# Kernel optimization log

Measured on AMD Instinct MI355X. Metric: run time of the kernel, lower is better.

Reference implementation:

```python
import jax, jax.numpy as jnp
import numpy as np

DIM = 64      # fixed by fuse=BasicConv2d(64,64)
HEADS = 8
B, H, W = 16, 128, 128
CPH = DIM // HEADS  # 8 channels per head


def conv2d(x, w, groups=1, pad=1):
    # x: [B,C,H,W], w: [O, C//groups, kh, kw]
    return jax.lax.conv_general_dilated(
        x, w, window_strides=(1, 1), padding=[(pad, pad), (pad, pad)],
        dimension_numbers=("NCHW", "OIHW", "NCHW"), feature_group_count=groups)


def setup_inputs() -> dict:
    key = jax.random.key(0)
    ks = jax.random.split(key, 8)
    y = jax.random.normal(ks[0], (B, DIM, H, W), jnp.float32)
    # conv3d kernels collapse to their middle depth slice (depth-1 input, zero pad)
    w_qkv = jax.random.normal(ks[1], (3 * DIM, DIM), jnp.float32) * 0.05        # 1x1x1 qkv
    w_dw = jax.random.normal(ks[2], (3 * DIM, 1, 3, 3), jnp.float32) * 0.1      # depthwise 3x3
    w_proj = jax.random.normal(ks[3], (DIM, DIM), jnp.float32) * 0.05           # 1x1x1 project_out
    w_fc = jax.random.normal(ks[4], (9, 3 * HEADS), jnp.float32) * 0.1          # fc: 24->9
    b_fc = jnp.zeros((9,), jnp.float32)
    w_dep = jax.random.normal(ks[5], (DIM, 9, 3, 3), jnp.float32) * 0.1         # grouped: 72->64, groups=8
    b_dep = jnp.zeros((DIM,), jnp.float32)
    temperature = jnp.ones((HEADS, 1, 1), jnp.float32)
    w_fuse = jax.random.normal(ks[6], (DIM, DIM, 3, 3), jnp.float32) * 0.05     # fuse conv, no bias
    bn_gamma = jnp.ones((DIM,), jnp.float32)
    bn_beta = jnp.zeros((DIM,), jnp.float32)
    bn_mean = jnp.zeros((DIM,), jnp.float32)
    bn_var = jnp.ones((DIM,), jnp.float32)
    return dict(y=y, w_qkv=w_qkv, w_dw=w_dw, w_proj=w_proj, w_fc=w_fc, b_fc=b_fc,
                w_dep=w_dep, b_dep=b_dep, temperature=temperature, w_fuse=w_fuse,
                bn_gamma=bn_gamma, bn_beta=bn_beta, bn_mean=bn_mean, bn_var=bn_var)


def reference(y, w_qkv, w_dw, w_proj, w_fc, b_fc, w_dep, b_dep, temperature,
              w_fuse, bn_gamma, bn_beta, bn_mean, bn_var):
    b, c, h, w = y.shape
    # qkv 1x1 conv then 3x3 depthwise conv (groups = 3*DIM)
    qkv = jnp.einsum('oc,bchw->bohw', w_qkv, y)                 # [b,192,h,w]
    qkv = conv2d(qkv, w_dw, groups=3 * DIM, pad=1)
    # dynamic kernel generation branch: flat reshape (row-major, matches torch)
    f_all = qkv.reshape(b, h * w, 3 * HEADS, CPH).transpose(0, 2, 1, 3)  # [b,24,hw,8]
    f_all = jnp.einsum('oc,bcne->bone', w_fc, f_all) + b_fc[None, :, None, None]  # [b,9,hw,8]
    f_conv = f_all.transpose(0, 3, 1, 2).reshape(b, 9 * CPH, h, w)       # [b,72,h,w]
    out_conv = conv2d(f_conv, w_dep, groups=CPH, pad=1) + b_dep[None, :, None, None]
    # channel (transposed) attention with L2-normalize + temperature + softmax
    q, k, v = jnp.split(qkv, 3, axis=1)
    def to_heads(t):
        return t.reshape(b, HEADS, CPH, h * w)
    q, k, v = to_heads(q), to_heads(k), to_heads(v)
    q = q / jnp.maximum(jnp.linalg.norm(q, axis=-1, keepdims=True), 1e-12)
    k = k / jnp.maximum(jnp.linalg.norm(k, axis=-1, keepdims=True), 1e-12)
    attn = jnp.einsum('bhcn,bhdn->bhcd', q, k) * temperature[None]       # [b,8,8,8]
    attn = jax.nn.softmax(attn, axis=-1)
    out = jnp.einsum('bhcd,bhdn->bhcn', attn, v).reshape(b, DIM, h, w)
    out = jnp.einsum('oc,bchw->bohw', w_proj, out)
    output = out + out_conv
    # fuse: conv3x3 (no bias) + BatchNorm (inference stats), then residual + ReLU
    fused = conv2d(output, w_fuse, pad=1)
    scale = (bn_gamma / jnp.sqrt(bn_var + 1e-5))[None, :, None, None]
    fused = (fused - bn_mean[None, :, None, None]) * scale + bn_beta[None, :, None, None]
    return jax.nn.relu(fused + y)
```

## Files before the change

### kernel.cpp

```cpp
#include <hip/hip_runtime.h>
#include <hip/hip_bf16.h>

#define BN 16
#define CC 64
#define HH 128
#define WW 128
#define HW 16384
#define C3 192
#define NHEADS 8


__global__ __launch_bounds__(256) void k_qkv1(const float* __restrict__ y,
                                              const float* __restrict__ w_qkv,
                                              float* __restrict__ out, int chunk) {
    __shared__ float ws[64 * 64];
    int tid = threadIdx.x;
    for (int i = tid; i < 4096; i += 256) {
        int c = i >> 6, o = i & 63;
        ws[i] = w_qkv[(chunk * 64 + o) * 64 + c];
    }
    __syncthreads();
    int bid = blockIdx.x;
    int b = bid >> 6;
    int ptile = bid & 63;
    int pxg = tid & 127;
    int osub = tid >> 7;
    int p0 = ptile * 256 + pxg * 2;
    const float* yb = y + (size_t)b * CC * HW + p0;
    float acc0[32];
    float acc1[32];
#pragma unroll
    for (int o = 0; o < 32; ++o) { acc0[o] = 0.f; acc1[o] = 0.f; }
    for (int c = 0; c < 64; ++c) {
        float2 yv = *(const float2*)(yb + (size_t)c * HW);
        const float* wr = &ws[c * 64 + osub * 32];
#pragma unroll
        for (int o = 0; o < 32; ++o) {
            float w = wr[o];
            acc0[o] = fmaf(w, yv.x, acc0[o]);
            acc1[o] = fmaf(w, yv.y, acc1[o]);
        }
    }
    float* ob = out + (size_t)b * 64 * HW + (size_t)(osub * 32) * HW + p0;
#pragma unroll
    for (int o = 0; o < 32; ++o) {
        *(float2*)(ob + (size_t)o * HW) = make_float2(acc0[o], acc1[o]);
    }
}

__global__ __launch_bounds__(256) void k_dw(const float* __restrict__ in,
                                            const float* __restrict__ w_dw,
                                            float* __restrict__ out, int chunk) {
    int bid = blockIdx.x;
    int tid = threadIdx.x;
    int b = bid >> 11;
    int rem = bid & 2047;
    int ch = rem >> 5;
    int tile = rem & 31;
    int pp = tile * 512 + tid * 2;
    int py = pp >> 7, px = pp & 127;
    const float* ib = in + ((size_t)b * 64 + ch) * HW;
    const float* wr = w_dw + (chunk * 64 + ch) * 9;
    float w[9];
#pragma unroll
    for (int i = 0; i < 9; ++i) w[i] = wr[i];
    float a0 = 0.f, a1 = 0.f;
#pragma unroll
    for (int ky = 0; ky < 3; ++ky) {
        int yy = py + ky - 1;
        bool yok = (unsigned)yy < 128u;
#pragma unroll
        for (int kx = 0; kx < 4; ++kx) {
            int xx = px + kx - 1;
            bool ok = yok && ((unsigned)xx < 128u);
            float v = ok ? ib[yy * 128 + xx] : 0.f;
            if (kx < 3) a0 = fmaf(w[ky * 3 + kx], v, a0);
            if (kx > 0) a1 = fmaf(w[ky * 3 + kx - 1], v, a1);
        }
    }
    *(float2*)(out + ((size_t)b * C3 + chunk * 64 + ch) * HW + pp) = make_float2(a0, a1);
}

__global__ __launch_bounds__(256) void k_fc(const float* __restrict__ qkv,
                                            const float* __restrict__ w_fc,
                                            const float* __restrict__ b_fc,
                                            float* __restrict__ fconv) {
    __shared__ float wf[216];
    __shared__ float bf[9];
    int tid = threadIdx.x;
    if (tid < 216) wf[tid] = w_fc[tid];
    if (tid < 9) bf[tid] = b_fc[tid];
    __syncthreads();
    int bid = blockIdx.x;
    int b = bid >> 9;
    int rem = bid & 511;
    int n = rem * 32 + (tid >> 3);
    int e = tid & 7;
    const float* x = qkv + (size_t)b * C3 * HW + (size_t)n * 192 + e;
    float xe[24];
#pragma unroll
    for (int g = 0; g < 24; ++g) xe[g] = x[g * 8];
    float* ob = fconv + (size_t)b * 72 * HW + n;
#pragma unroll
    for (int o = 0; o < 9; ++o) {
        float acc = bf[o];
#pragma unroll
        for (int g = 0; g < 24; ++g) acc = fmaf(wf[o * 24 + g], xe[g], acc);
        ob[(size_t)(e * 9 + o) * HW] = acc;
    }
}

#define GST 20
__global__ __launch_bounds__(256) void k_gconv(const float* __restrict__ fconv,
                                               const float* __restrict__ w_dep,
                                               const float* __restrict__ b_dep,
                                               float* __restrict__ outO) {
    __shared__ __align__(16) float sm_in[9 * 18 * GST];
    __shared__ __align__(16) float sm_w[81 * 8];
    __shared__ float sm_b[8];
    int tid = threadIdx.x;
    int bid = blockIdx.x;
    int b = bid >> 9;
    int rem = bid & 511;
    int grp = rem >> 6;
    int tile = rem & 63;
    int ty0 = (tile >> 3) * 16, tx0 = (tile & 7) * 16;
    const float* ibase = fconv + ((size_t)b * 72 + grp * 9) * HW;
    for (int i = tid; i < 9 * 324; i += 256) {
        int c = i / 324;
        int r2 = i - c * 324;
        int r = r2 / 18;
        int q = r2 - r * 18;
        int yy = ty0 + r - 1, xx = tx0 + q - 1;
        sm_in[c * (18 * GST) + r * GST + q] =
            ((unsigned)yy < 128u && (unsigned)xx < 128u)
                ? ibase[(size_t)c * HW + yy * 128 + xx] : 0.f;
    }
    for (int i = tid; i < 648; i += 256) {
        int o = i & 7;
        int ik = i >> 3;
        sm_w[i] = w_dep[(size_t)(grp * 8 + o) * 81 + ik];
    }
    if (tid < 8) sm_b[tid] = b_dep[grp * 8 + tid];
    __syncthreads();
    int row = tid >> 4, col = tid & 15;
    float acc[8];
#pragma unroll
    for (int o = 0; o < 8; ++o) acc[o] = sm_b[o];
#pragma unroll
    for (int ic = 0; ic < 9; ++ic) {
        float nb[3][3];
        const float* sc = &sm_in[ic * (18 * GST) + row * GST + col];
#pragma unroll
        for (int r = 0; r < 3; ++r)
#pragma unroll
            for (int q = 0; q < 3; ++q) nb[r][q] = sc[r * GST + q];
        const float* wp = &sm_w[ic * 72];
#pragma unroll
        for (int k = 0; k < 9; ++k) {
            float4 w0 = *(const float4*)(wp + k * 8);
            float4 w1 = *(const float4*)(wp + k * 8 + 4);
            float v = nb[k / 3][k % 3];
            acc[0] = fmaf(w0.x, v, acc[0]);
            acc[1] = fmaf(w0.y, v, acc[1]);
            acc[2] = fmaf(w0.z, v, acc[2]);
            acc[3] = fmaf(w0.w, v, acc[3]);
            acc[4] = fmaf(w1.x, v, acc[4]);
            acc[5] = fmaf(w1.y, v, acc[5]);
            acc[6] = fmaf(w1.z, v, acc[6]);
            acc[7] = fmaf(w1.w, v, acc[7]);
        }
    }
    float* ob = outO + ((size_t)b * 64 + grp * 8) * HW + (ty0 + row) * 128 + tx0 + col;
#pragma unroll
    for (int o = 0; o < 8; ++o) ob[(size_t)o * HW] = acc[o];
}

__global__ __launch_bounds__(256) void k_attn(const float* __restrict__ qkv,
                                              const float* __restrict__ temperature,
                                              float* __restrict__ attn) {
    __shared__ float red[4][64];
    __shared__ float redq[4][8];
    __shared__ float redk[4][8];
    __shared__ float sm_inv[16];
    __shared__ float lg[64];
    int bid = blockIdx.x;
    int b = bid >> 3, h = bid & 7;
    int tid = threadIdx.x;
    const float* Q = qkv + ((size_t)b * C3 + h * 8) * HW;
    const float* K = Q + (size_t)64 * HW;
    float acc[64], qs[8], ks[8];
#pragma unroll
    for (int j = 0; j < 64; ++j) acc[j] = 0.f;
#pragma unroll
    for (int d = 0; d < 8; ++d) { qs[d] = 0.f; ks[d] = 0.f; }
    for (int i = tid; i < HW; i += 256) {
        float qv[8], kv[8];
#pragma unroll
        for (int d = 0; d < 8; ++d) {
            qv[d] = Q[(size_t)d * HW + i];
            kv[d] = K[(size_t)d * HW + i];
        }
#pragma unroll
        for (int d = 0; d < 8; ++d) {
            qs[d] = fmaf(qv[d], qv[d], qs[d]);
            ks[d] = fmaf(kv[d], kv[d], ks[d]);
        }
#pragma unroll
        for (int c = 0; c < 8; ++c)
#pragma unroll
            for (int d = 0; d < 8; ++d)
                acc[c * 8 + d] = fmaf(qv[c], kv[d], acc[c * 8 + d]);
    }
#pragma unroll
    for (int j = 0; j < 64; ++j) {
#pragma unroll
        for (int off = 32; off; off >>= 1) acc[j] += __shfl_down(acc[j], off, 64);
    }
#pragma unroll
    for (int d = 0; d < 8; ++d) {
#pragma unroll
        for (int off = 32; off; off >>= 1) {
            qs[d] += __shfl_down(qs[d], off, 64);
            ks[d] += __shfl_down(ks[d], off, 64);
        }
    }
    int lane = tid & 63, wv = tid >> 6;
    if (lane == 0) {
#pragma unroll
        for (int j = 0; j < 64; ++j) red[wv][j] = acc[j];
#pragma unroll
        for (int d = 0; d < 8; ++d) { redq[wv][d] = qs[d]; redk[wv][d] = ks[d]; }
    }
    __syncthreads();
    if (tid < 16) {
        int d = tid & 7;
        float s = (tid < 8) ? (redq[0][d] + redq[1][d] + redq[2][d] + redq[3][d])
                            : (redk[0][d] + redk[1][d] + redk[2][d] + redk[3][d]);
        sm_inv[tid] = 1.f / fmaxf(sqrtf(s), 1e-12f);
    }
    __syncthreads();
    if (tid < 64) {
        float s = red[0][tid] + red[1][tid] + red[2][tid] + red[3][tid];
        int c = tid >> 3, d = tid & 7;
        lg[tid] = s * sm_inv[c] * sm_inv[8 + d] * temperature[h];
    }
    __syncthreads();
    if (tid < 8) {
        int c = tid;
        float m = lg[c * 8];
#pragma unroll
        for (int d = 1; d < 8; ++d) m = fmaxf(m, lg[c * 8 + d]);
        float ssum = 0.f, ex[8];
#pragma unroll
        for (int d = 0; d < 8; ++d) { ex[d] = expf(lg[c * 8 + d] - m); ssum += ex[d]; }
        float inv = 1.f / ssum;
#pragma unroll
        for (int d = 0; d < 8; ++d)
            attn[((size_t)(b * 8 + h) * 8 + c) * 8 + d] = ex[d] * inv;
    }
}

__global__ __launch_bounds__(256) void k_av_proj(const float* __restrict__ qkv,
                                                 const float* __restrict__ attn,
                                                 const float* __restrict__ w_proj,
                                                 float* __restrict__ outO) {
    __shared__ float at[512];
    __shared__ float wp[4096];
    int tid = threadIdx.x;
    int bid = blockIdx.x;
    int b = bid >> 6, tile = bid & 63;
    for (int i = tid; i < 512; i += 256) at[i] = attn[b * 512 + i];
    for (int i = tid; i < 4096; i += 256) {
        int c = i >> 6, o = i & 63;
        wp[i] = w_proj[o * 64 + c];
    }
    __syncthreads();
    int p = tile * 256 + tid;
    const float* vb = qkv + ((size_t)b * C3 + 128) * HW + p;
    float av[64];
#pragma unroll
    for (int h = 0; h < 8; ++h) {
        float vv[8];
#pragma unroll
        for (int d = 0; d < 8; ++d) vv[d] = vb[(size_t)(h * 8 + d) * HW];
#pragma unroll
        for (int ci = 0; ci < 8; ++ci) {
            float s = 0.f;
#pragma unroll
            for (int d = 0; d < 8; ++d) s = fmaf(at[(h * 8 + ci) * 8 + d], vv[d], s);
            av[h * 8 + ci] = s;
        }
    }
    float* ob = outO + (size_t)b * 64 * HW + p;
    float acc[64];
#pragma unroll
    for (int o = 0; o < 64; ++o) acc[o] = ob[(size_t)o * HW];
    for (int c = 0; c < 64; ++c) {
        float a = av[c];
        const float* wr = &wp[c * 64];
#pragma unroll
        for (int o = 0; o < 64; ++o) acc[o] = fmaf(wr[o], a, acc[o]);
    }
#pragma unroll
    for (int o = 0; o < 64; ++o) ob[(size_t)o * HW] = acc[o];
}

#define ST 20
__global__ __launch_bounds__(256) void k_fuse(const float* __restrict__ outO,
                                              const float* __restrict__ w_fuse,
                                              const float* __restrict__ bn_gamma,
                                              const float* __restrict__ bn_beta,
                                              const float* __restrict__ bn_mean,
                                              const float* __restrict__ bn_var,
                                              const float* __restrict__ y,
                                              float* __restrict__ dout) {
    __shared__ __align__(16) float sm_in[8 * 18 * ST];
    __shared__ __align__(16) float sm_w[8 * 9 * 64];
    __shared__ float sm_sc[64];
    __shared__ float sm_sb[64];
    int tid = threadIdx.x;
    int bid = blockIdx.x;
    int b = bid >> 6;
    int tile = bid & 63;
    int ty0 = (tile >> 3) * 16, tx0 = (tile & 7) * 16;

    if (tid < 64) {
        float sc = bn_gamma[tid] * rsqrtf(bn_var[tid] + 1e-5f);
        sm_sc[tid] = sc;
        sm_sb[tid] = bn_beta[tid] - bn_mean[tid] * sc;
    }

    int osub = tid >> 6;
    int o0 = osub * 16;
    int lane = tid & 63;
    int col = lane & 15;
    int rowg = lane >> 4;
    int r0 = rowg * 4;

    const float* ib = outO + (size_t)b * 64 * HW;
    float acc[4][16];
#pragma unroll
    for (int p = 0; p < 4; ++p)
#pragma unroll
        for (int o = 0; o < 16; ++o) acc[p][o] = 0.f;

    for (int ch = 0; ch < 8; ++ch) {
        int c0 = ch * 8;
        __syncthreads();
        for (int i = tid; i < 8 * 18 * 18; i += 256) {
            int c = i / 324;
            int rem = i - c * 324;
            int r = rem / 18;
            int q = rem - r * 18;
            int yy = ty0 + r - 1;
            int xx = tx0 + q - 1;
            float v = ((unsigned)yy < 128u && (unsigned)xx < 128u)
                          ? ib[(size_t)(c0 + c) * HW + yy * 128 + xx] : 0.f;
            sm_in[c * (18 * ST) + r * ST + q] = v;
        }
        for (int i = tid; i < 8 * 9 * 64; i += 256) {
            int o = i & 63;
            int kk = (i >> 6) % 9;
            int c = i / 576;
            sm_w[(c * 9 + kk) * 64 + o] = w_fuse[((size_t)o * 64 + (c0 + c)) * 9 + kk];
        }
        __syncthreads();
        for (int cc = 0; cc < 8; ++cc) {
            float nb[6][3];
            const float* sin_c = &sm_in[cc * (18 * ST)];
#pragma unroll
            for (int r = 0; r < 6; ++r)
#pragma unroll
                for (int q = 0; q < 3; ++q)
                    nb[r][q] = sin_c[(r0 + r) * ST + col + q];
            const float* wc = &sm_w[cc * 576 + o0];
#pragma unroll
            for (int k = 0; k < 9; ++k) {
                int ky = k / 3, kx = k % 3;
                float4 w0 = *(const float4*)(wc + k * 64);
                float4 w1 = *(const float4*)(wc + k * 64 + 4);
                float4 w2 = *(const float4*)(wc + k * 64 + 8);
                float4 w3 = *(const float4*)(wc + k * 64 + 12);
#pragma unroll
                for (int p = 0; p < 4; ++p) {
                    float v = nb[p + ky][kx];
                    acc[p][0]  = fmaf(w0.x, v, acc[p][0]);
                    acc[p][1]  = fmaf(w0.y, v, acc[p][1]);
                    acc[p][2]  = fmaf(w0.z, v, acc[p][2]);
                    acc[p][3]  = fmaf(w0.w, v, acc[p][3]);
                    acc[p][4]  = fmaf(w1.x, v, acc[p][4]);
                    acc[p][5]  = fmaf(w1.y, v, acc[p][5]);
                    acc[p][6]  = fmaf(w1.z, v, acc[p][6]);
                    acc[p][7]  = fmaf(w1.w, v, acc[p][7]);
                    acc[p][8]  = fmaf(w2.x, v, acc[p][8]);
                    acc[p][9]  = fmaf(w2.y, v, acc[p][9]);
                    acc[p][10] = fmaf(w2.z, v, acc[p][10]);
                    acc[p][11] = fmaf(w2.w, v, acc[p][11]);
                    acc[p][12] = fmaf(w3.x, v, acc[p][12]);
                    acc[p][13] = fmaf(w3.y, v, acc[p][13]);
                    acc[p][14] = fmaf(w3.z, v, acc[p][14]);
                    acc[p][15] = fmaf(w3.w, v, acc[p][15]);
                }
            }
        }
    }
#pragma unroll
    for (int o = 0; o < 16; ++o) {
        int og = o0 + o;
        float sc = sm_sc[og], sb = sm_sb[og];
#pragma unroll
        for (int p = 0; p < 4; ++p) {
            int pyy = ty0 + r0 + p;
            int pxx = tx0 + col;
            size_t idx = ((size_t)b * 64 + og) * HW + pyy * 128 + pxx;
            float v = acc[p][o] * sc + sb + y[idx];
            dout[idx] = fmaxf(v, 0.f);
        }
    }
}

extern "C" void kernel_launch(void* const* d_in, const int* in_sizes, int n_in,
                              void* d_out, int out_size, void* d_ws, size_t ws_size,
                              hipStream_t stream) {
    const float* y           = (const float*)d_in[0];
    const float* w_qkv       = (const float*)d_in[1];
    const float* w_dw        = (const float*)d_in[2];
    const float* w_proj      = (const float*)d_in[3];
    const float* w_fc        = (const float*)d_in[4];
    const float* b_fc        = (const float*)d_in[5];
    const float* w_dep       = (const float*)d_in[6];
    const float* b_dep       = (const float*)d_in[7];
    const float* temperature = (const float*)d_in[8];
    const float* w_fuse      = (const float*)d_in[9];
    const float* bn_gamma    = (const float*)d_in[10];
    const float* bn_beta     = (const float*)d_in[11];
    const float* bn_mean     = (const float*)d_in[12];
    const float* bn_var      = (const float*)d_in[13];
    float* out = (float*)d_out;

    float* ws    = (float*)d_ws;
    float* qkvB  = ws;
    float* bufT  = ws + 25165824;
    float* bufO  = ws + 34603008;
    float* attn  = ws + 42992640;
    (void)in_sizes; (void)n_in; (void)out_size; (void)ws_size;

    for (int g = 0; g < 2; ++g) {
        const float* yg = y + (size_t)g * 8 * CC * HW;
        float* outg = out + (size_t)g * 8 * CC * HW;
        for (int chunk = 0; chunk < 3; ++chunk) {
            k_qkv1<<<512, 256, 0, stream>>>(yg, w_qkv, bufT, chunk);
            k_dw<<<16384, 256, 0, stream>>>(bufT, w_dw, qkvB, chunk);
        }
        k_fc<<<4096, 256, 0, stream>>>(qkvB, w_fc, b_fc, bufT);
        k_gconv<<<4096, 256, 0, stream>>>(bufT, w_dep, b_dep, bufO);
        k_attn<<<64, 256, 0, stream>>>(qkvB, temperature, attn);
        k_av_proj<<<512, 256, 0, stream>>>(qkvB, attn, w_proj, bufO);
        k_fuse<<<512, 256, 0, stream>>>(bufO, w_fuse, bn_gamma, bn_beta,
                                        bn_mean, bn_var, yg, outg);
    }
}
```

Baseline: 1.045 ms.

## Stage fc input in LDS, split attention reduction, halve fuse output channels per block

k_fc now loads each block's 32 spatial rows of qkv into shared memory with coalesced float4 reads, then computes per-thread outputs from LDS instead of strided global loads. The attention Gram reduction is split into four spatial segments across 256 blocks, followed by a small finalize kernel, to raise parallelism beyond the previous 64 blocks. k_fuse assigns 32 output channels per block and doubles the grid, which cuts accumulator registers for higher occupancy at the cost of reloading the input tile twice.

```diff
diff --git a/kernel.cpp b/kernel.cpp
--- a/kernel.cpp
+++ b/kernel.cpp
@@ -87,27 +87,37 @@
                                             float* __restrict__ fconv) {
     __shared__ float wf[216];
     __shared__ float bf[9];
+    __shared__ float sx[32 * 193];
     int tid = threadIdx.x;
     if (tid < 216) wf[tid] = w_fc[tid];
     if (tid < 9) bf[tid] = b_fc[tid];
-    __syncthreads();
     int bid = blockIdx.x;
     int b = bid >> 9;
-    int rem = bid & 511;
-    int n = rem * 32 + (tid >> 3);
-    int e = tid & 7;
-    const float* x = qkv + (size_t)b * C3 * HW + (size_t)n * 192 + e;
-    float xe[24];
-#pragma unroll
-    for (int g = 0; g < 24; ++g) xe[g] = x[g * 8];
-    float* ob = fconv + (size_t)b * 72 * HW + n;
-#pragma unroll
-    for (int o = 0; o < 9; ++o) {
-        float acc = bf[o];
-#pragma unroll
-        for (int g = 0; g < 24; ++g) acc = fmaf(wf[o * 24 + g], xe[g], acc);
-        ob[(size_t)(e * 9 + o) * HW] = acc;
-    }
+    int n0 = (bid & 511) * 32;
+    const float* src = qkv + (size_t)b * C3 * HW + (size_t)n0 * 192;
+    for (int f4 = tid; f4 < 1536; f4 += 256) {
+        int f = f4 * 4;
+        int nl = f / 192;
+        int r = f - nl * 192;
+        float4 v = *(const float4*)(src + f);
+        float* d = &sx[nl * 193 + r];
+        d[0] = v.x; d[1] = v.y; d[2] = v.z; d[3] = v.w;
+    }
+    __syncthreads();
+    int e = tid >> 5, n = tid & 31;
+    const float* xr = &sx[n * 193 + e];
+    float acc[9];
+#pragma unroll
+    for (int o = 0; o < 9; ++o) acc[o] = bf[o];
+#pragma unroll
+    for (int g = 0; g < 24; ++g) {
+        float xv = xr[g * 8];
+#pragma unroll
+        for (int o = 0; o < 9; ++o) acc[o] = fmaf(wf[o * 24 + g], xv, acc[o]);
+    }
+    float* ob = fconv + (size_t)b * 72 * HW + n0 + n;
+#pragma unroll
+    for (int o = 0; o < 9; ++o) ob[(size_t)(e * 9 + o) * HW] = acc[o];
 }
 
 #define GST 20
@@ -176,16 +186,13 @@
     for (int o = 0; o < 8; ++o) ob[(size_t)o * HW] = acc[o];
 }
 
-__global__ __launch_bounds__(256) void k_attn(const float* __restrict__ qkv,
-                                              const float* __restrict__ temperature,
-                                              float* __restrict__ attn) {
+__global__ __launch_bounds__(256) void k_attn_p(const float* __restrict__ qkv,
+                                                float* __restrict__ partial) {
     __shared__ float red[4][64];
     __shared__ float redq[4][8];
     __shared__ float redk[4][8];
-    __shared__ float sm_inv[16];
-    __shared__ float lg[64];
-    int bid = blockIdx.x;
-    int b = bid >> 3, h = bid & 7;
+    int bid = blockIdx.x;
+    int b = bid >> 5, h = (bid >> 2) & 7, seg = bid & 3;
     int tid = threadIdx.x;
     const float* Q = qkv + ((size_t)b * C3 + h * 8) * HW;
     const float* K = Q + (size_t)64 * HW;
@@ -194,7 +201,8 @@
     for (int j = 0; j < 64; ++j) acc[j] = 0.f;
 #pragma unroll
     for (int d = 0; d < 8; ++d) { qs[d] = 0.f; ks[d] = 0.f; }
-    for (int i = tid; i < HW; i += 256) {
+    int iend = (seg + 1) * 4096;
+    for (int i = seg * 4096 + tid; i < iend; i += 256) {
         float qv[8], kv[8];
 #pragma unroll
         for (int d = 0; d < 8; ++d) {
@@ -233,17 +241,36 @@
         for (int d = 0; d < 8; ++d) { redq[wv][d] = qs[d]; redk[wv][d] = ks[d]; }
     }
     __syncthreads();
-    if (tid < 16) {
-        int d = tid & 7;
-        float s = (tid < 8) ? (redq[0][d] + redq[1][d] + redq[2][d] + redq[3][d])
-                            : (redk[0][d] + redk[1][d] + redk[2][d] + redk[3][d]);
-        sm_inv[tid] = 1.f / fmaxf(sqrtf(s), 1e-12f);
-    }
-    __syncthreads();
+    float* outp = partial + (size_t)bid * 80;
     if (tid < 64) {
-        float s = red[0][tid] + red[1][tid] + red[2][tid] + red[3][tid];
+        outp[tid] = red[0][tid] + red[1][tid] + red[2][tid] + red[3][tid];
+    } else if (tid < 72) {
+        int d = tid - 64;
+        outp[64 + d] = redq[0][d] + redq[1][d] + redq[2][d] + redq[3][d];
+    } else if (tid < 80) {
+        int d = tid - 72;
+        outp[72 + d] = redk[0][d] + redk[1][d] + redk[2][d] + redk[3][d];
+    }
+}
+
+__global__ __launch_bounds__(256) void k_attn_f(const float* __restrict__ partial,
+                                                const float* __restrict__ temperature,
+                                                float* __restrict__ attn) {
+    __shared__ float sm[80];
+    __shared__ float lg[64];
+    int bh = blockIdx.x;
+    int h = bh & 7;
+    int tid = threadIdx.x;
+    if (tid < 80) {
+        const float* pp = partial + (size_t)bh * 4 * 80 + tid;
+        sm[tid] = pp[0] + pp[80] + pp[160] + pp[240];
+    }
+    __syncthreads();
+    if (tid < 64) {
         int c = tid >> 3, d = tid & 7;
-        lg[tid] = s * sm_inv[c] * sm_inv[8 + d] * temperature[h];
+        float invq = 1.f / fmaxf(sqrtf(sm[64 + c]), 1e-12f);
+        float invk = 1.f / fmaxf(sqrtf(sm[72 + d]), 1e-12f);
+        lg[tid] = sm[tid] * invq * invk * temperature[h];
     }
     __syncthreads();
     if (tid < 8) {
@@ -257,7 +284,7 @@
         float inv = 1.f / ssum;
 #pragma unroll
         for (int d = 0; d < 8; ++d)
-            attn[((size_t)(b * 8 + h) * 8 + c) * 8 + d] = ex[d] * inv;
+            attn[(size_t)bh * 64 + c * 8 + d] = ex[d] * inv;
     }
 }
 
@@ -316,13 +343,15 @@
                                               const float* __restrict__ y,
                                               float* __restrict__ dout) {
     __shared__ __align__(16) float sm_in[8 * 18 * ST];
-    __shared__ __align__(16) float sm_w[8 * 9 * 64];
+    __shared__ __align__(16) float sm_w[8 * 9 * 32];
     __shared__ float sm_sc[64];
     __shared__ float sm_sb[64];
     int tid = threadIdx.x;
     int bid = blockIdx.x;
-    int b = bid >> 6;
-    int tile = bid & 63;
+    int b = bid >> 7;
+    int rem = bid & 127;
+    int ob32 = rem >> 6;
+    int tile = rem & 63;
     int ty0 = (tile >> 3) * 16, tx0 = (tile & 7) * 16;
 
     if (tid < 64) {
@@ -332,38 +361,39 @@
     }
 
     int osub = tid >> 6;
-    int o0 = osub * 16;
+    int o0 = osub * 8;
     int lane = tid & 63;
     int col = lane & 15;
     int rowg = lane >> 4;
     int r0 = rowg * 4;
 
     const float* ib = outO + (size_t)b * 64 * HW;
-    float acc[4][16];
+    float acc[4][8];
 #pragma unroll
     for (int p = 0; p < 4; ++p)
 #pragma unroll
-        for (int o = 0; o < 16; ++o) acc[p][o] = 0.f;
+        for (int o = 0; o < 8; ++o) acc[p][o] = 0.f;
 
     for (int ch = 0; ch < 8; ++ch) {
         int c0 = ch * 8;
         __syncthreads();
         for (int i = tid; i < 8 * 18 * 18; i += 256) {
             int c = i / 324;
-            int rem = i - c * 324;
-            int r = rem / 18;
-            int q = rem - r * 18;
+            int rem2 = i - c * 324;
+            int r = rem2 / 18;
+            int q = rem2 - r * 18;
             int yy = ty0 + r - 1;
             int xx = tx0 + q - 1;
             float v = ((unsigned)yy < 128u && (unsigned)xx < 128u)
                           ? ib[(size_t)(c0 + c) * HW + yy * 128 + xx] : 0.f;
             sm_in[c * (18 * ST) + r * ST + q] = v;
         }
-        for (int i = tid; i < 8 * 9 * 64; i += 256) {
-            int o = i & 63;
-            int kk = (i >> 6) % 9;
-            int c = i / 576;
-            sm_w[(c * 9 + kk) * 64 + o] = w_fuse[((size_t)o * 64 + (c0 + c)) * 9 + kk];
+        for (int i = tid; i < 8 * 9 * 32; i += 256) {
+            int o = i & 31;
+            int kk = (i >> 5) % 9;
+            int c = i / 288;
+            sm_w[(c * 9 + kk) * 32 + o] =
+                w_fuse[((size_t)(ob32 * 32 + o) * 64 + (c0 + c)) * 9 + kk];
         }
         __syncthreads();
         for (int cc = 0; cc < 8; ++cc) {
@@ -374,40 +404,30 @@
 #pragma unroll
                 for (int q = 0; q < 3; ++q)
                     nb[r][q] = sin_c[(r0 + r) * ST + col + q];
-            const float* wc = &sm_w[cc * 576 + o0];
+            const float* wc = &sm_w[cc * 288 + o0];
 #pragma unroll
             for (int k = 0; k < 9; ++k) {
                 int ky = k / 3, kx = k % 3;
-                float4 w0 = *(const float4*)(wc + k * 64);
-                float4 w1 = *(const float4*)(wc + k * 64 + 4);
-                float4 w2 = *(const float4*)(wc + k * 64 + 8);
-                float4 w3 = *(const float4*)(wc + k * 64 + 12);
+                float4 w0 = *(const float4*)(wc + k * 32);
+                float4 w1 = *(const float4*)(wc + k * 32 + 4);
 #pragma unroll
                 for (int p = 0; p < 4; ++p) {
                     float v = nb[p + ky][kx];
-                    acc[p][0]  = fmaf(w0.x, v, acc[p][0]);
-                    acc[p][1]  = fmaf(w0.y, v, acc[p][1]);
-                    acc[p][2]  = fmaf(w0.z, v, acc[p][2]);
-                    acc[p][3]  = fmaf(w0.w, v, acc[p][3]);
-                    acc[p][4]  = fmaf(w1.x, v, acc[p][4]);
-                    acc[p][5]  = fmaf(w1.y, v, acc[p][5]);
-                    acc[p][6]  = fmaf(w1.z, v, acc[p][6]);
-                    acc[p][7]  = fmaf(w1.w, v, acc[p][7]);
-                    acc[p][8]  = fmaf(w2.x, v, acc[p][8]);
-                    acc[p][9]  = fmaf(w2.y, v, acc[p][9]);
-                    acc[p][10] = fmaf(w2.z, v, acc[p][10]);
-                    acc[p][11] = fmaf(w2.w, v, acc[p][11]);
-                    acc[p][12] = fmaf(w3.x, v, acc[p][12]);
-                    acc[p][13] = fmaf(w3.y, v, acc[p][13]);
-                    acc[p][14] = fmaf(w3.z, v, acc[p][14]);
-                    acc[p][15] = fmaf(w3.w, v, acc[p][15]);
+                    acc[p][0] = fmaf(w0.x, v, acc[p][0]);
+                    acc[p][1] = fmaf(w0.y, v, acc[p][1]);
+                    acc[p][2] = fmaf(w0.z, v, acc[p][2]);
+                    acc[p][3] = fmaf(w0.w, v, acc[p][3]);
+                    acc[p][4] = fmaf(w1.x, v, acc[p][4]);
+                    acc[p][5] = fmaf(w1.y, v, acc[p][5]);
+                    acc[p][6] = fmaf(w1.z, v, acc[p][6]);
+                    acc[p][7] = fmaf(w1.w, v, acc[p][7]);
                 }
             }
         }
     }
 #pragma unroll
-    for (int o = 0; o < 16; ++o) {
-        int og = o0 + o;
+    for (int o = 0; o < 8; ++o) {
+        int og = ob32 * 32 + o0 + o;
         float sc = sm_sc[og], sb = sm_sb[og];
 #pragma unroll
         for (int p = 0; p < 4; ++p) {
@@ -444,6 +464,7 @@
     float* bufT  = ws + 25165824;
     float* bufO  = ws + 34603008;
     float* attn  = ws + 42992640;
+    float* attnP = ws + 42996736;
     (void)in_sizes; (void)n_in; (void)out_size; (void)ws_size;
 
     for (int g = 0; g < 2; ++g) {
@@ -455,9 +476,10 @@
         }
         k_fc<<<4096, 256, 0, stream>>>(qkvB, w_fc, b_fc, bufT);
         k_gconv<<<4096, 256, 0, stream>>>(bufT, w_dep, b_dep, bufO);
-        k_attn<<<64, 256, 0, stream>>>(qkvB, temperature, attn);
+        k_attn_p<<<256, 256, 0, stream>>>(qkvB, attnP);
+        k_attn_f<<<64, 256, 0, stream>>>(attnP, temperature, attn);
         k_av_proj<<<512, 256, 0, stream>>>(qkvB, attn, w_proj, bufO);
-        k_fuse<<<512, 256, 0, stream>>>(bufO, w_fuse, bn_gamma, bn_beta,
-                                        bn_mean, bn_var, yg, outg);
-    }
-}
+        k_fuse<<<1024, 256, 0, stream>>>(bufO, w_fuse, bn_gamma, bn_beta,
+                                         bn_mean, bn_var, yg, outg);
+    }
+}
```

Result: no change. 1.025 ms (-1.9%).
